# Kernel tuning notes

Hardware: AMD Instinct MI355X
Metric: run time of the kernel (lower is better)

Reference implementation:

```python
import jax, jax.numpy as jnp
import numpy as np

B, H, CI, O = 8, 16, 16, 16          # batch, child spatial, child caps, parent caps
K, S, ROUTINGS = 3, 1, 3             # kernel, stride, EM iterations
FINAL_LAMBDA = 0.01
EPS = 1e-9


def setup_inputs() -> dict:
    key = jax.random.key(0)
    k1, k2, k3, k4, k5 = jax.random.split(key, 5)
    inputs_pose = jax.random.normal(k1, (B, H, H, CI, 16), dtype=jnp.float32)
    inputs_activation = jax.random.uniform(k2, (B, H, H, CI, 1), dtype=jnp.float32)
    # transformation matrices: [1, k*k*child_caps, parent_caps, 4, 4]
    w = jax.random.normal(k3, (1, K * K * CI, O, 4, 4), dtype=jnp.float32)
    beta_a = jax.random.normal(k4, (O,), dtype=jnp.float32)
    beta_v = jax.random.normal(k5, (O,), dtype=jnp.float32)
    return {"inputs_pose": inputs_pose, "inputs_activation": inputs_activation,
            "w": w, "beta_a": beta_a, "beta_v": beta_v}


def _extract_patches(x, k, s):
    # kernel_tile: im2col-like gather. x: [B, H, W, ...] -> [B, p, p, k, k, ...]
    Hs = x.shape[1]
    p = (Hs - k) // s + 1
    idx = (jnp.arange(p) * s)[:, None] + jnp.arange(k)[None, :]      # [p, k]
    xh = x[:, idx]                   # [B, ph, kh, W, ...]
    patches = xh[:, :, :, idx]       # [B, ph, kh, pw, kw, ...]
    return jnp.swapaxes(patches, 2, 3), p


def _child_index_map(Hs, k, s, p):
    # flat child spatial index feeding each (parent pos, kernel slot)
    ph = np.arange(p)[:, None] * s + np.arange(k)[None, :]           # [p, k]
    ch = ph[:, None, :, None] * Hs + ph[None, :, None, :]            # [p, p, k, k]
    return ch.reshape(p * p, k * k)                                   # [P2, K2]


def reference(inputs_pose, inputs_activation, w, beta_a, beta_v):
    P = (H - K) // S + 1
    P2, K2 = P * P, K * K
    K2CI = K2 * CI

    # ---- kernel_tile ----
    pose_t, _ = _extract_patches(inputs_pose, K, S)       # [B,P,P,K,K,CI,16]
    act_t, _ = _extract_patches(inputs_activation, K, S)  # [B,P,P,K,K,CI,1]
    pose_unroll = pose_t.reshape(B * P2, K2CI, 4, 4)
    act_unroll = act_t.reshape(B * P2, K2CI)

    # ---- compute_votes: tiny 4x4 matmuls per (child slot, parent cap) ----
    votes = jnp.einsum('nkpq,koqr->nkopr', pose_unroll, w[0])  # [B*P2,K2CI,O,4,4]
    votes = votes.reshape(B, P2, K2CI, O, 16)
    act_i = act_unroll.reshape(B, P2, K2CI, 1, 1)

    # ---- spatial routing bookkeeping (static integers) ----
    child_idx = _child_index_map(H, K, S, P)                    # [P2, K2]
    kk_child = np.repeat(child_idx, CI, axis=1)                 # [P2, K2CI]
    counts = np.zeros(H * H, np.float32)
    np.add.at(counts, child_idx.reshape(-1), 1.0)               # parents per child pos
    cap_id = np.tile(np.arange(CI), K2)                         # [K2CI]
    seg = jnp.asarray((kk_child * CI + cap_id[None, :]).reshape(-1))  # [P2*K2CI]
    n_seg = H * H * CI

    # initial routing: uniform over all (parent pos, parent cap) each child feeds
    rr0 = 1.0 / (O * counts[kk_child])                          # [P2, K2CI]
    rr = jnp.asarray(rr0)[None, :, :, None, None]               # bcast [1,P2,K2CI,1,1]

    beta_a_b = beta_a.reshape(1, 1, 1, O, 1)
    beta_v_b = beta_v.reshape(1, 1, 1, O, 1)

    mean = act_j = None
    for it in range(ROUTINGS):
        inv_temp = FINAL_LAMBDA * (1.0 - 0.95 ** (it + 1))
        # ---- M-step: weighted Gaussian statistics ----
        rr_prime = rr * act_i                                   # [B,P2,K2CI,O,1]
        rr_sum = jnp.sum(rr_prime, axis=2, keepdims=True) + EPS # [B,P2,1,O,1]
        mean = jnp.sum(rr_prime * votes, axis=2, keepdims=True) / rr_sum
        var = jnp.sum(rr_prime * jnp.square(votes - mean), axis=2, keepdims=True) / rr_sum + EPS
        cost_h = (beta_v_b + 0.5 * jnp.log(var)) * rr_sum       # [B,P2,1,O,16]
        cost = jnp.sum(cost_h, axis=-1, keepdims=True)          # [B,P2,1,O,1]
        act_j = jax.nn.sigmoid(inv_temp * (beta_a_b - cost))    # [B,P2,1,O,1]
        # ---- E-step: softmax over all (parent pos, parent cap) per child capsule ----
        if it < ROUTINGS - 1:
            log_p = -0.5 * jnp.sum(jnp.square(votes - mean) / var
                                   + jnp.log(2.0 * np.pi * var), axis=-1)  # [B,P2,K2CI,O]
            zz = jnp.log(act_j[..., 0] + EPS) + log_p           # [B,P2,K2CI,O]
            z = jnp.transpose(zz, (1, 2, 0, 3)).reshape(P2 * K2CI, B, O)
            row_max = jnp.max(z, axis=-1)                       # [P2*K2CI, B]
            seg_max = jax.ops.segment_max(row_max, seg, num_segments=n_seg)
            g = seg_max[seg][..., None]
            ez = jnp.exp(z - g)
            denom = jax.ops.segment_sum(jnp.sum(ez, axis=-1), seg, num_segments=n_seg)[seg]
            rr_new = ez / (denom[..., None] + EPS)              # sums to 1 per child capsule
            rr = jnp.transpose(rr_new.reshape(P2, K2CI, B, O), (2, 0, 1, 3))[..., None]

    pose_out = mean[:, :, 0].reshape(B, P, P, O, 16)
    act_out = act_j[:, :, 0].reshape(B, P, P, O, 1)
    return pose_out, act_out
```

## Files before the change

kernel.cpp:

```cpp
#include <hip/hip_runtime.h>

namespace {
constexpr int B_ = 8, H_ = 16, CI_ = 16, O_ = 16, P_ = 14;
constexpr int P2_ = P_ * P_;
constexpr int K2CI_ = 144;
constexpr int NV_ = 2304;
constexpr float EPS_ = 1e-9f;
constexpr float LOG2PI_ = 1.8378770664093453f;

using f2 = __attribute__((ext_vector_type(2))) float;

__device__ __forceinline__ float cnt1(int h) {
  int lo = (h - (P_ - 1)) > 0 ? (h - (P_ - 1)) : 0;
  int hi = h < 2 ? h : 2;
  return (float)(hi - lo + 1);
}

__global__ __launch_bounds__(256) void transpose_w(const float* __restrict__ w,
                                                   float* __restrict__ wt) {
  const int i = blockIdx.x * 256 + threadIdx.x;
  const int ko = i >> 4, q = (i >> 2) & 3, r = i & 3;
  wt[(ko << 4) + (r << 2) + q] = w[i];
}

template <int MODE>
__global__ __launch_bounds__(512, 4) void caps_main(
    const float* __restrict__ pose, const float* __restrict__ act,
    const float* __restrict__ wt, const float* __restrict__ beta_a,
    const float* __restrict__ beta_v, const float* __restrict__ zin,
    const float* __restrict__ gmax, const float* __restrict__ gden,
    float* __restrict__ zout, float* __restrict__ out) {
  __shared__ __align__(16) float pose_s[NV_];
  __shared__ float rr_s[(MODE == 0) ? K2CI_ : NV_];
  __shared__ f2 partv[4][512];
  __shared__ float partr[512];
  __shared__ f2 sfin[4][64];
  __shared__ float sfr[64];
  __shared__ float gm_s[(MODE == 0) ? 1 : K2CI_];
  __shared__ float ad_s[(MODE == 0) ? 1 : K2CI_];

  const int tid = threadIdx.x;
  const int wv = __builtin_amdgcn_readfirstlane(tid >> 6);
  const int l = tid & 63;
  const int o = l >> 2, r = l & 3;
  const int pid = blockIdx.x;
  const int b = pid / P2_;
  const int p2 = pid - b * P2_;
  const int pi = p2 / P_;
  const int pj = p2 - pi * P_;
  const float inv_temp = (MODE == 0) ? 0.0005f : (MODE == 1) ? 0.000975f : 0.00142625f;

  if (tid < K2CI_) {
    const int ci = tid & 15, kk = tid >> 4;
    const int ki = (kk >= 6) ? 2 : (kk >= 3) ? 1 : 0, kj = kk - 3 * ki;
    const float* src = pose + ((size_t)((b * H_ + pi + ki) * H_ + pj + kj) << 8) + (ci << 4);
    const float4 R0 = *(const float4*)(src);
    const float4 R1 = *(const float4*)(src + 4);
    const float4 R2 = *(const float4*)(src + 8);
    const float4 R3 = *(const float4*)(src + 12);
    float4* dst = (float4*)(pose_s + (kk << 8) + (ci << 4));
    dst[0] = make_float4(R0.x, R1.x, R2.x, R3.x);
    dst[1] = make_float4(R0.y, R1.y, R2.y, R3.y);
    dst[2] = make_float4(R0.z, R1.z, R2.z, R3.z);
    dst[3] = make_float4(R0.w, R1.w, R2.w, R3.w);

    const int cidx = ((b * H_ + pi + ki) * H_ + pj + kj) * CI_ + ci;
    if (MODE == 0) {
      rr_s[tid] = act[cidx] / (16.0f * cnt1(pi + ki) * cnt1(pj + kj));
    } else {
      gm_s[tid] = gmax[cidx];
      ad_s[tid] = act[cidx] / (gden[cidx] + EPS_);
    }
  }
  if (MODE != 0) {
    __syncthreads();
    for (int i4 = tid; i4 < NV_ / 4; i4 += 512) {
      const float4 z4 = ((const float4*)(zin + (size_t)pid * NV_))[i4];
      const int k = i4 >> 2;
      const float gmk = gm_s[k], adk = ad_s[k];
      float4 r4;
      r4.x = __expf(z4.x - gmk) * adk;
      r4.y = __expf(z4.y - gmk) * adk;
      r4.z = __expf(z4.z - gmk) * adk;
      r4.w = __expf(z4.w - gmk) * adk;
      ((float4*)rr_s)[i4] = r4;
    }
  }
  __syncthreads();

  const float bvo = 16.0f * beta_v[o];
  const float bao = beta_a[o];

  const float* wt_l = wt + (l << 2);
  const int ci0 = wv * 2;

#define WT_OFF(idx) ((((idx) >> 1) << 12) + ((ci0 + ((idx)&1)) << 8))
#define PB_OFF(idx) ((((idx) >> 1) << 8) + ((ci0 + ((idx)&1)) << 4))

  f2 vc01[18], vc23[18];
  float prr = 0.f;
  f2 pm01 = {0.f, 0.f}, pm23 = {0.f, 0.f}, pv01 = {0.f, 0.f}, pv23 = {0.f, 0.f};
  {
    float4 wbuf0 = *(const float4*)(wt_l + WT_OFF(0));
    float4 wbuf1 = *(const float4*)(wt_l + WT_OFF(1));
#pragma unroll
    for (int idx = 0; idx < 18; ++idx) {
      const float4 w4 = (idx & 1) ? wbuf1 : wbuf0;
      if (idx < 16) {
        if (idx & 1)
          wbuf1 = *(const float4*)(wt_l + WT_OFF(idx + 2));
        else
          wbuf0 = *(const float4*)(wt_l + WT_OFF(idx + 2));
      }
      const float* pb = pose_s + PB_OFF(idx);
      const float4 P0 = *(const float4*)(pb);
      const float4 P1 = *(const float4*)(pb + 4);
      const float4 P2 = *(const float4*)(pb + 8);
      const float4 P3 = *(const float4*)(pb + 12);
      f2 v01 = (f2){P0.x, P0.y} * w4.x;
      f2 v23 = (f2){P0.z, P0.w} * w4.x;
      v01 = __builtin_elementwise_fma((f2){P1.x, P1.y}, (f2){w4.y, w4.y}, v01);
      v23 = __builtin_elementwise_fma((f2){P1.z, P1.w}, (f2){w4.y, w4.y}, v23);
      v01 = __builtin_elementwise_fma((f2){P2.x, P2.y}, (f2){w4.z, w4.z}, v01);
      v23 = __builtin_elementwise_fma((f2){P2.z, P2.w}, (f2){w4.z, w4.z}, v23);
      v01 = __builtin_elementwise_fma((f2){P3.x, P3.y}, (f2){w4.w, w4.w}, v01);
      v23 = __builtin_elementwise_fma((f2){P3.z, P3.w}, (f2){w4.w, w4.w}, v23);
      if (MODE != 2) {
        vc01[idx] = v01;
        vc23[idx] = v23;
      }
      const int k = ((idx >> 1) << 4) + ci0 + (idx & 1);
      const float rrk = (MODE == 0) ? rr_s[k] : rr_s[(k << 4) + o];
      prr += rrk;
      const f2 rr2 = {rrk, rrk};
      const f2 a01 = rr2 * v01, a23 = rr2 * v23;
      pm01 += a01;
      pm23 += a23;
      pv01 = __builtin_elementwise_fma(a01, v01, pv01);
      pv23 = __builtin_elementwise_fma(a23, v23, pv23);
    }
  }
  partv[0][tid] = pm01; partv[1][tid] = pm23;
  partv[2][tid] = pv01; partv[3][tid] = pv23;
  partr[tid] = prr;
  __syncthreads();
  if (tid < 320) {
    if (tid < 256) {
      const int st = tid >> 6, li = tid & 63;
      f2 acc = partv[st][li];
#pragma unroll
      for (int wvi = 1; wvi < 8; ++wvi) acc += partv[st][wvi * 64 + li];
      sfin[st][li] = acc;
    } else {
      const int li = tid & 63;
      float acc = partr[li];
#pragma unroll
      for (int wvi = 1; wvi < 8; ++wvi) acc += partr[wvi * 64 + li];
      sfr[li] = acc;
    }
  }
  __syncthreads();
  const f2 S01 = sfin[0][l], S23 = sfin[1][l];
  const f2 V01 = sfin[2][l], V23 = sfin[3][l];
  const float rsum = sfr[l] + EPS_;
  const float irs = 1.0f / rsum;
  const f2 irs2 = {irs, irs};
  const f2 m01 = S01 * irs2, m23 = S23 * irs2;
  const f2 zero2 = {0.f, 0.f}, eps2 = {EPS_, EPS_};
  const f2 va01 = __builtin_elementwise_max(V01 * irs2 - m01 * m01, zero2) + eps2;
  const f2 va23 = __builtin_elementwise_max(V23 * irs2 - m23 * m23, zero2) + eps2;
  float slv = __logf(va01.x) + __logf(va01.y) + __logf(va23.x) + __logf(va23.y);
  slv += __shfl_xor(slv, 1);
  slv += __shfl_xor(slv, 2);
  const float cost = (bvo + 0.5f * slv) * rsum;
  const float aj = 1.0f / (1.0f + __expf(-inv_temp * (bao - cost)));

  if (MODE == 2) {
    if (wv == 0) {
      float* ob = out + ((size_t)(pid * 16 + o) << 4) + r;
      ob[0] = m01.x; ob[4] = m01.y; ob[8] = m23.x; ob[12] = m23.y;
      if (r == 0) out[(size_t)B_ * P2_ * O_ * 16 + pid * 16 + o] = aj;
    }
    return;
  }

  const f2 iv01 = {1.0f / va01.x, 1.0f / va01.y};
  const f2 iv23 = {1.0f / va23.x, 1.0f / va23.y};
  const float Cz = __logf(aj + EPS_) - 0.5f * (slv + 16.0f * LOG2PI_);
  float* zo = zout + (size_t)pid * NV_ + o;
  {
#pragma unroll
    for (int idx = 0; idx < 18; ++idx) {
      const f2 d01 = vc01[idx] - m01, d23 = vc23[idx] - m23;
      const f2 q2 = __builtin_elementwise_fma(d01 * d01, iv01, (d23 * d23) * iv23);
      float q = q2.x + q2.y;
      q += __shfl_xor(q, 1);
      q += __shfl_xor(q, 2);
      const int k = ((idx >> 1) << 4) + ci0 + (idx & 1);
      if (r == 0) zo[k << 4] = Cz - 0.5f * q;
    }
  }
#undef WT_OFF
#undef PB_OFF
}

__global__ __launch_bounds__(256) void seg_reduce(const float* __restrict__ z,
                                                  float* __restrict__ gmax,
                                                  float* __restrict__ gden) {
  const int tid = blockIdx.x * 256 + threadIdx.x;
  const int part = tid & 3, ci = (tid >> 2) & 15, w2 = (tid >> 6) & 15;
  const int h = (tid >> 10) & 15, b = tid >> 14;
  float4 v[9];
  float m = -3.0e38f;
#pragma unroll
  for (int s = 0; s < 9; ++s) {
    const int ki = (s >= 6) ? 2 : (s >= 3) ? 1 : 0, kj = s - 3 * ki;
    const int pi = h - ki, pj = w2 - kj;
    if ((unsigned)pi < (unsigned)P_ && (unsigned)pj < (unsigned)P_) {
      v[s] = *(const float4*)(z + (size_t)(b * P2_ + pi * P_ + pj) * NV_ + s * 256 +
                              ci * 16 + part * 4);
    } else {
      v[s] = make_float4(-3.0e38f, -3.0e38f, -3.0e38f, -3.0e38f);
    }
    m = fmaxf(m, fmaxf(fmaxf(v[s].x, v[s].y), fmaxf(v[s].z, v[s].w)));
  }
  m = fmaxf(m, __shfl_xor(m, 1));
  m = fmaxf(m, __shfl_xor(m, 2));
  float s_ = 0.f;
#pragma unroll
  for (int s = 0; s < 9; ++s) {
    s_ += __expf(v[s].x - m) + __expf(v[s].y - m) + __expf(v[s].z - m) + __expf(v[s].w - m);
  }
  s_ += __shfl_xor(s_, 1);
  s_ += __shfl_xor(s_, 2);
  if (part == 0) {
    gmax[tid >> 2] = m;
    gden[tid >> 2] = s_;
  }
}
}

extern "C" void kernel_launch(void* const* d_in, const int* in_sizes, int n_in,
                              void* d_out, int out_size, void* d_ws, size_t ws_size,
                              hipStream_t stream) {
  const float* pose = (const float*)d_in[0];
  const float* act = (const float*)d_in[1];
  const float* w = (const float*)d_in[2];
  const float* ba = (const float*)d_in[3];
  const float* bv = (const float*)d_in[4];
  float* out = (float*)d_out;

  float* z = (float*)d_ws;
  float* gm = z + (size_t)B_ * P2_ * NV_;
  float* gd = gm + B_ * H_ * H_ * CI_;
  float* wt = gd + B_ * H_ * H_ * CI_;

  const int NB = B_ * P2_;
  transpose_w<<<144, 256, 0, stream>>>(w, wt);
  caps_main<0><<<NB, 512, 0, stream>>>(pose, act, wt, ba, bv, z, gm, gd, z, out);
  seg_reduce<<<512, 256, 0, stream>>>(z, gm, gd);
  caps_main<1><<<NB, 512, 0, stream>>>(pose, act, wt, ba, bv, z, gm, gd, z, out);
  seg_reduce<<<512, 256, 0, stream>>>(z, gm, gd);
  caps_main<2><<<NB, 512, 0, stream>>>(pose, act, wt, ba, bv, z, gm, gd, z, out);
}
```

Baseline: 153.6 us.

## Pre-transpose pose in global memory and read it directly instead of staging in LDS

Adds a pose transpose to the existing weight-transpose kernel so the 4x4 pose matrices are stored transposed in workspace once. The main kernels then drop the per-block LDS staging of the 3x3 patch and load pose directly from global memory (using an asm-forced VGPR offset so the loads stay per-lane vector loads). The weight prefetch is also deepened from two to four buffers. This removes the LDS footprint and the staging work at the cost of an extra global pass over pose and more global/cache traffic inside the inner loop.

```diff
diff --git a/kernel.cpp b/kernel.cpp
--- a/kernel.cpp
+++ b/kernel.cpp
@@ -3,6 +3,7 @@
 namespace {
 constexpr int B_ = 8, H_ = 16, CI_ = 16, O_ = 16, P_ = 14;
 constexpr int P2_ = P_ * P_;
+constexpr int NB_ = B_ * P2_;
 constexpr int K2CI_ = 144;
 constexpr int NV_ = 2304;
 constexpr float EPS_ = 1e-9f;
@@ -16,21 +17,29 @@
   return (float)(hi - lo + 1);
 }
 
-__global__ __launch_bounds__(256) void transpose_w(const float* __restrict__ w,
-                                                   float* __restrict__ wt) {
-  const int i = blockIdx.x * 256 + threadIdx.x;
-  const int ko = i >> 4, q = (i >> 2) & 3, r = i & 3;
-  wt[(ko << 4) + (r << 2) + q] = w[i];
+__global__ __launch_bounds__(256) void transpose_all(const float* __restrict__ pose,
+                                                     float* __restrict__ pose_t,
+                                                     const float* __restrict__ w,
+                                                     float* __restrict__ wt) {
+  if (blockIdx.x < 2048) {
+    const int i = blockIdx.x * 256 + threadIdx.x;
+    const int cell = i >> 4, idx = i & 15;
+    const int p = idx >> 2, q = idx & 3;
+    pose_t[(cell << 4) + (q << 2) + p] = pose[i];
+  } else {
+    const int i = (blockIdx.x - 2048) * 256 + threadIdx.x;
+    const int ko = i >> 4, q = (i >> 2) & 3, r = i & 3;
+    wt[(ko << 4) + (r << 2) + q] = w[i];
+  }
 }
 
 template <int MODE>
 __global__ __launch_bounds__(512, 4) void caps_main(
-    const float* __restrict__ pose, const float* __restrict__ act,
+    const float* __restrict__ pose_t, const float* __restrict__ act,
     const float* __restrict__ wt, const float* __restrict__ beta_a,
     const float* __restrict__ beta_v, const float* __restrict__ zin,
     const float* __restrict__ gmax, const float* __restrict__ gden,
     float* __restrict__ zout, float* __restrict__ out) {
-  __shared__ __align__(16) float pose_s[NV_];
   __shared__ float rr_s[(MODE == 0) ? K2CI_ : NV_];
   __shared__ f2 partv[4][512];
   __shared__ float partr[512];
@@ -53,17 +62,6 @@
   if (tid < K2CI_) {
     const int ci = tid & 15, kk = tid >> 4;
     const int ki = (kk >= 6) ? 2 : (kk >= 3) ? 1 : 0, kj = kk - 3 * ki;
-    const float* src = pose + ((size_t)((b * H_ + pi + ki) * H_ + pj + kj) << 8) + (ci << 4);
-    const float4 R0 = *(const float4*)(src);
-    const float4 R1 = *(const float4*)(src + 4);
-    const float4 R2 = *(const float4*)(src + 8);
-    const float4 R3 = *(const float4*)(src + 12);
-    float4* dst = (float4*)(pose_s + (kk << 8) + (ci << 4));
-    dst[0] = make_float4(R0.x, R1.x, R2.x, R3.x);
-    dst[1] = make_float4(R0.y, R1.y, R2.y, R3.y);
-    dst[2] = make_float4(R0.z, R1.z, R2.z, R3.z);
-    dst[3] = make_float4(R0.w, R1.w, R2.w, R3.w);
-
     const int cidx = ((b * H_ + pi + ki) * H_ + pj + kj) * CI_ + ci;
     if (MODE == 0) {
       rr_s[tid] = act[cidx] / (16.0f * cnt1(pi + ki) * cnt1(pj + kj));
@@ -91,28 +89,27 @@
   const float bvo = 16.0f * beta_v[o];
   const float bao = beta_a[o];
 
+  int vofs;
+  asm volatile("v_mov_b32 %0, 0" : "=v"(vofs));
+  const float* pose_b = pose_t + ((size_t)((b * H_ + pi) * H_ + pj) << 8) + vofs;
   const float* wt_l = wt + (l << 2);
   const int ci0 = wv * 2;
 
 #define WT_OFF(idx) ((((idx) >> 1) << 12) + ((ci0 + ((idx)&1)) << 8))
-#define PB_OFF(idx) ((((idx) >> 1) << 8) + ((ci0 + ((idx)&1)) << 4))
+#define PB_OFF(idx) (((((idx) >> 1) / 3) << 12) + ((((idx) >> 1) % 3) << 8) + ((ci0 + ((idx)&1)) << 4))
 
   f2 vc01[18], vc23[18];
   float prr = 0.f;
   f2 pm01 = {0.f, 0.f}, pm23 = {0.f, 0.f}, pv01 = {0.f, 0.f}, pv23 = {0.f, 0.f};
   {
-    float4 wbuf0 = *(const float4*)(wt_l + WT_OFF(0));
-    float4 wbuf1 = *(const float4*)(wt_l + WT_OFF(1));
+    float4 wbuf[4];
+#pragma unroll
+    for (int j = 0; j < 4; ++j) wbuf[j] = *(const float4*)(wt_l + WT_OFF(j));
 #pragma unroll
     for (int idx = 0; idx < 18; ++idx) {
-      const float4 w4 = (idx & 1) ? wbuf1 : wbuf0;
-      if (idx < 16) {
-        if (idx & 1)
-          wbuf1 = *(const float4*)(wt_l + WT_OFF(idx + 2));
-        else
-          wbuf0 = *(const float4*)(wt_l + WT_OFF(idx + 2));
-      }
-      const float* pb = pose_s + PB_OFF(idx);
+      const float4 w4 = wbuf[idx & 3];
+      if (idx < 14) wbuf[idx & 3] = *(const float4*)(wt_l + WT_OFF(idx + 4));
+      const float* pb = pose_b + PB_OFF(idx);
       const float4 P0 = *(const float4*)(pb);
       const float4 P1 = *(const float4*)(pb + 4);
       const float4 P2 = *(const float4*)(pb + 8);
@@ -251,15 +248,15 @@
   float* out = (float*)d_out;
 
   float* z = (float*)d_ws;
-  float* gm = z + (size_t)B_ * P2_ * NV_;
+  float* gm = z + (size_t)NB_ * NV_;
   float* gd = gm + B_ * H_ * H_ * CI_;
   float* wt = gd + B_ * H_ * H_ * CI_;
-
-  const int NB = B_ * P2_;
-  transpose_w<<<144, 256, 0, stream>>>(w, wt);
-  caps_main<0><<<NB, 512, 0, stream>>>(pose, act, wt, ba, bv, z, gm, gd, z, out);
+  float* pt = wt + 36864;
+
+  transpose_all<<<2192, 256, 0, stream>>>(pose, pt, w, wt);
+  caps_main<0><<<NB_, 512, 0, stream>>>(pt, act, wt, ba, bv, z, gm, gd, z, out);
   seg_reduce<<<512, 256, 0, stream>>>(z, gm, gd);
-  caps_main<1><<<NB, 512, 0, stream>>>(pose, act, wt, ba, bv, z, gm, gd, z, out);
+  caps_main<1><<<NB_, 512, 0, stream>>>(pt, act, wt, ba, bv, z, gm, gd, z, out);
   seg_reduce<<<512, 256, 0, stream>>>(z, gm, gd);
-  caps_main<2><<<NB, 512, 0, stream>>>(pose, act, wt, ba, bv, z, gm, gd, z, out);
-}
+  caps_main<2><<<NB_, 512, 0, stream>>>(pt, act, wt, ba, bv, z, gm, gd, z, out);
+}
```

Result: slower. 212.8 us (+38.6%).

## Fuse all routing stages into one cooperative persistent kernel with grid syncs

Applied to the files above, without the earlier changes.

Merges the weight transpose, three EM routing passes and two segment reductions into a single cooperative kernel. Stages are separated by grid.sync instead of kernel launches, and blocks loop persistently over parent positions. This removes launch gaps between six kernels. In exchange it adds grid-wide barrier cost, sizes shared memory for the worst case across all modes, and may lower occupancy because the grid is capped by the co-resident block count.

```diff
diff --git a/kernel.cpp b/kernel.cpp
--- a/kernel.cpp
+++ b/kernel.cpp
@@ -1,14 +1,30 @@
 #include <hip/hip_runtime.h>
+#include <hip/hip_cooperative_groups.h>
+
+namespace cg = cooperative_groups;
 
 namespace {
 constexpr int B_ = 8, H_ = 16, CI_ = 16, O_ = 16, P_ = 14;
 constexpr int P2_ = P_ * P_;
+constexpr int NB_ = B_ * P2_;
 constexpr int K2CI_ = 144;
 constexpr int NV_ = 2304;
+constexpr int NSEG_ = B_ * H_ * H_ * CI_;
 constexpr float EPS_ = 1e-9f;
 constexpr float LOG2PI_ = 1.8378770664093453f;
 
 using f2 = __attribute__((ext_vector_type(2))) float;
+
+struct __align__(16) Smem {
+  float pose_s[NV_];
+  float rr_s[NV_];
+  f2 partv[4][512];
+  float partr[512];
+  f2 sfin[4][64];
+  float sfr[64];
+  float gm_s[K2CI_];
+  float ad_s[K2CI_];
+};
 
 __device__ __forceinline__ float cnt1(int h) {
   int lo = (h - (P_ - 1)) > 0 ? (h - (P_ - 1)) : 0;
@@ -16,34 +32,17 @@
   return (float)(hi - lo + 1);
 }
 
-__global__ __launch_bounds__(256) void transpose_w(const float* __restrict__ w,
-                                                   float* __restrict__ wt) {
-  const int i = blockIdx.x * 256 + threadIdx.x;
-  const int ko = i >> 4, q = (i >> 2) & 3, r = i & 3;
-  wt[(ko << 4) + (r << 2) + q] = w[i];
-}
-
 template <int MODE>
-__global__ __launch_bounds__(512, 4) void caps_main(
+__device__ __forceinline__ void caps_body(
+    const int pid, const int tid, Smem& sm,
     const float* __restrict__ pose, const float* __restrict__ act,
     const float* __restrict__ wt, const float* __restrict__ beta_a,
-    const float* __restrict__ beta_v, const float* __restrict__ zin,
+    const float* __restrict__ beta_v, float* __restrict__ z,
     const float* __restrict__ gmax, const float* __restrict__ gden,
-    float* __restrict__ zout, float* __restrict__ out) {
-  __shared__ __align__(16) float pose_s[NV_];
-  __shared__ float rr_s[(MODE == 0) ? K2CI_ : NV_];
-  __shared__ f2 partv[4][512];
-  __shared__ float partr[512];
-  __shared__ f2 sfin[4][64];
-  __shared__ float sfr[64];
-  __shared__ float gm_s[(MODE == 0) ? 1 : K2CI_];
-  __shared__ float ad_s[(MODE == 0) ? 1 : K2CI_];
-
-  const int tid = threadIdx.x;
+    float* __restrict__ out) {
   const int wv = __builtin_amdgcn_readfirstlane(tid >> 6);
   const int l = tid & 63;
   const int o = l >> 2, r = l & 3;
-  const int pid = blockIdx.x;
   const int b = pid / P2_;
   const int p2 = pid - b * P2_;
   const int pi = p2 / P_;
@@ -58,7 +57,7 @@
     const float4 R1 = *(const float4*)(src + 4);
     const float4 R2 = *(const float4*)(src + 8);
     const float4 R3 = *(const float4*)(src + 12);
-    float4* dst = (float4*)(pose_s + (kk << 8) + (ci << 4));
+    float4* dst = (float4*)(sm.pose_s + (kk << 8) + (ci << 4));
     dst[0] = make_float4(R0.x, R1.x, R2.x, R3.x);
     dst[1] = make_float4(R0.y, R1.y, R2.y, R3.y);
     dst[2] = make_float4(R0.z, R1.z, R2.z, R3.z);
@@ -66,24 +65,24 @@
 
     const int cidx = ((b * H_ + pi + ki) * H_ + pj + kj) * CI_ + ci;
     if (MODE == 0) {
-      rr_s[tid] = act[cidx] / (16.0f * cnt1(pi + ki) * cnt1(pj + kj));
+      sm.rr_s[tid] = act[cidx] / (16.0f * cnt1(pi + ki) * cnt1(pj + kj));
     } else {
-      gm_s[tid] = gmax[cidx];
-      ad_s[tid] = act[cidx] / (gden[cidx] + EPS_);
+      sm.gm_s[tid] = gmax[cidx];
+      sm.ad_s[tid] = act[cidx] / (gden[cidx] + EPS_);
     }
   }
   if (MODE != 0) {
     __syncthreads();
     for (int i4 = tid; i4 < NV_ / 4; i4 += 512) {
-      const float4 z4 = ((const float4*)(zin + (size_t)pid * NV_))[i4];
+      const float4 z4 = ((const float4*)(z + (size_t)pid * NV_))[i4];
       const int k = i4 >> 2;
-      const float gmk = gm_s[k], adk = ad_s[k];
+      const float gmk = sm.gm_s[k], adk = sm.ad_s[k];
       float4 r4;
       r4.x = __expf(z4.x - gmk) * adk;
       r4.y = __expf(z4.y - gmk) * adk;
       r4.z = __expf(z4.z - gmk) * adk;
       r4.w = __expf(z4.w - gmk) * adk;
-      ((float4*)rr_s)[i4] = r4;
+      ((float4*)sm.rr_s)[i4] = r4;
     }
   }
   __syncthreads();
@@ -112,7 +111,7 @@
         else
           wbuf0 = *(const float4*)(wt_l + WT_OFF(idx + 2));
       }
-      const float* pb = pose_s + PB_OFF(idx);
+      const float* pb = sm.pose_s + PB_OFF(idx);
       const float4 P0 = *(const float4*)(pb);
       const float4 P1 = *(const float4*)(pb + 4);
       const float4 P2 = *(const float4*)(pb + 8);
@@ -130,7 +129,7 @@
         vc23[idx] = v23;
       }
       const int k = ((idx >> 1) << 4) + ci0 + (idx & 1);
-      const float rrk = (MODE == 0) ? rr_s[k] : rr_s[(k << 4) + o];
+      const float rrk = (MODE == 0) ? sm.rr_s[k] : sm.rr_s[(k << 4) + o];
       prr += rrk;
       const f2 rr2 = {rrk, rrk};
       const f2 a01 = rr2 * v01, a23 = rr2 * v23;
@@ -140,29 +139,29 @@
       pv23 = __builtin_elementwise_fma(a23, v23, pv23);
     }
   }
-  partv[0][tid] = pm01; partv[1][tid] = pm23;
-  partv[2][tid] = pv01; partv[3][tid] = pv23;
-  partr[tid] = prr;
+  sm.partv[0][tid] = pm01; sm.partv[1][tid] = pm23;
+  sm.partv[2][tid] = pv01; sm.partv[3][tid] = pv23;
+  sm.partr[tid] = prr;
   __syncthreads();
   if (tid < 320) {
     if (tid < 256) {
       const int st = tid >> 6, li = tid & 63;
-      f2 acc = partv[st][li];
-#pragma unroll
-      for (int wvi = 1; wvi < 8; ++wvi) acc += partv[st][wvi * 64 + li];
-      sfin[st][li] = acc;
+      f2 acc = sm.partv[st][li];
+#pragma unroll
+      for (int wvi = 1; wvi < 8; ++wvi) acc += sm.partv[st][wvi * 64 + li];
+      sm.sfin[st][li] = acc;
     } else {
       const int li = tid & 63;
-      float acc = partr[li];
-#pragma unroll
-      for (int wvi = 1; wvi < 8; ++wvi) acc += partr[wvi * 64 + li];
-      sfr[li] = acc;
+      float acc = sm.partr[li];
+#pragma unroll
+      for (int wvi = 1; wvi < 8; ++wvi) acc += sm.partr[wvi * 64 + li];
+      sm.sfr[li] = acc;
     }
   }
   __syncthreads();
-  const f2 S01 = sfin[0][l], S23 = sfin[1][l];
-  const f2 V01 = sfin[2][l], V23 = sfin[3][l];
-  const float rsum = sfr[l] + EPS_;
+  const f2 S01 = sm.sfin[0][l], S23 = sm.sfin[1][l];
+  const f2 V01 = sm.sfin[2][l], V23 = sm.sfin[3][l];
+  const float rsum = sm.sfr[l] + EPS_;
   const float irs = 1.0f / rsum;
   const f2 irs2 = {irs, irs};
   const f2 m01 = S01 * irs2, m23 = S23 * irs2;
@@ -181,14 +180,11 @@
       ob[0] = m01.x; ob[4] = m01.y; ob[8] = m23.x; ob[12] = m23.y;
       if (r == 0) out[(size_t)B_ * P2_ * O_ * 16 + pid * 16 + o] = aj;
     }
-    return;
-  }
-
-  const f2 iv01 = {1.0f / va01.x, 1.0f / va01.y};
-  const f2 iv23 = {1.0f / va23.x, 1.0f / va23.y};
-  const float Cz = __logf(aj + EPS_) - 0.5f * (slv + 16.0f * LOG2PI_);
-  float* zo = zout + (size_t)pid * NV_ + o;
-  {
+  } else {
+    const f2 iv01 = {1.0f / va01.x, 1.0f / va01.y};
+    const f2 iv23 = {1.0f / va23.x, 1.0f / va23.y};
+    const float Cz = __logf(aj + EPS_) - 0.5f * (slv + 16.0f * LOG2PI_);
+    float* zo = z + (size_t)pid * NV_ + o;
 #pragma unroll
     for (int idx = 0; idx < 18; ++idx) {
       const f2 d01 = vc01[idx] - m01, d23 = vc23[idx] - m23;
@@ -204,38 +200,88 @@
 #undef PB_OFF
 }
 
-__global__ __launch_bounds__(256) void seg_reduce(const float* __restrict__ z,
-                                                  float* __restrict__ gmax,
-                                                  float* __restrict__ gden) {
-  const int tid = blockIdx.x * 256 + threadIdx.x;
-  const int part = tid & 3, ci = (tid >> 2) & 15, w2 = (tid >> 6) & 15;
-  const int h = (tid >> 10) & 15, b = tid >> 14;
-  float4 v[9];
-  float m = -3.0e38f;
-#pragma unroll
-  for (int s = 0; s < 9; ++s) {
-    const int ki = (s >= 6) ? 2 : (s >= 3) ? 1 : 0, kj = s - 3 * ki;
-    const int pi = h - ki, pj = w2 - kj;
-    if ((unsigned)pi < (unsigned)P_ && (unsigned)pj < (unsigned)P_) {
-      v[s] = *(const float4*)(z + (size_t)(b * P2_ + pi * P_ + pj) * NV_ + s * 256 +
-                              ci * 16 + part * 4);
-    } else {
-      v[s] = make_float4(-3.0e38f, -3.0e38f, -3.0e38f, -3.0e38f);
-    }
-    m = fmaxf(m, fmaxf(fmaxf(v[s].x, v[s].y), fmaxf(v[s].z, v[s].w)));
-  }
-  m = fmaxf(m, __shfl_xor(m, 1));
-  m = fmaxf(m, __shfl_xor(m, 2));
-  float s_ = 0.f;
-#pragma unroll
-  for (int s = 0; s < 9; ++s) {
-    s_ += __expf(v[s].x - m) + __expf(v[s].y - m) + __expf(v[s].z - m) + __expf(v[s].w - m);
-  }
-  s_ += __shfl_xor(s_, 1);
-  s_ += __shfl_xor(s_, 2);
-  if (part == 0) {
-    gmax[tid >> 2] = m;
-    gden[tid >> 2] = s_;
+__device__ __forceinline__ void seg_body(const int gtid, const int gstride,
+                                         const float* __restrict__ z,
+                                         float* __restrict__ gmax,
+                                         float* __restrict__ gden) {
+  for (int t = gtid; t < NSEG_ * 4; t += gstride) {
+    const int part = t & 3, ci = (t >> 2) & 15, w2 = (t >> 6) & 15;
+    const int h = (t >> 10) & 15, b = t >> 14;
+    float4 v[9];
+    float m = -3.0e38f;
+#pragma unroll
+    for (int s = 0; s < 9; ++s) {
+      const int ki = (s >= 6) ? 2 : (s >= 3) ? 1 : 0, kj = s - 3 * ki;
+      const int pi = h - ki, pj = w2 - kj;
+      if ((unsigned)pi < (unsigned)P_ && (unsigned)pj < (unsigned)P_) {
+        v[s] = *(const float4*)(z + (size_t)(b * P2_ + pi * P_ + pj) * NV_ + s * 256 +
+                                ci * 16 + part * 4);
+      } else {
+        v[s] = make_float4(-3.0e38f, -3.0e38f, -3.0e38f, -3.0e38f);
+      }
+      m = fmaxf(m, fmaxf(fmaxf(v[s].x, v[s].y), fmaxf(v[s].z, v[s].w)));
+    }
+    m = fmaxf(m, __shfl_xor(m, 1));
+    m = fmaxf(m, __shfl_xor(m, 2));
+    float s_ = 0.f;
+#pragma unroll
+    for (int s = 0; s < 9; ++s) {
+      s_ += __expf(v[s].x - m) + __expf(v[s].y - m) + __expf(v[s].z - m) + __expf(v[s].w - m);
+    }
+    s_ += __shfl_xor(s_, 1);
+    s_ += __shfl_xor(s_, 2);
+    if (part == 0) {
+      gmax[t >> 2] = m;
+      gden[t >> 2] = s_;
+    }
+  }
+}
+
+__global__ __launch_bounds__(512, 4) void caps_fused(
+    const float* __restrict__ pose, const float* __restrict__ act,
+    const float* __restrict__ w, const float* __restrict__ beta_a,
+    const float* __restrict__ beta_v, float* __restrict__ z,
+    float* __restrict__ gm, float* __restrict__ gd,
+    float* __restrict__ wt, float* __restrict__ out) {
+  __shared__ Smem sm;
+  const int tid = threadIdx.x;
+  cg::grid_group grid = cg::this_grid();
+  const int G = gridDim.x;
+  const int gtid = blockIdx.x * 512 + tid;
+  const int gstride = G * 512;
+
+  for (int i = gtid; i < K2CI_ * O_ * 16; i += gstride) {
+    const int ko = i >> 4, q = (i >> 2) & 3, r = i & 3;
+    wt[(ko << 4) + (r << 2) + q] = w[i];
+  }
+  __threadfence();
+  grid.sync();
+
+  for (int pid = blockIdx.x; pid < NB_; pid += G) {
+    caps_body<0>(pid, tid, sm, pose, act, wt, beta_a, beta_v, z, gm, gd, out);
+    __syncthreads();
+  }
+  __threadfence();
+  grid.sync();
+
+  seg_body(gtid, gstride, z, gm, gd);
+  __threadfence();
+  grid.sync();
+
+  for (int pid = blockIdx.x; pid < NB_; pid += G) {
+    caps_body<1>(pid, tid, sm, pose, act, wt, beta_a, beta_v, z, gm, gd, out);
+    __syncthreads();
+  }
+  __threadfence();
+  grid.sync();
+
+  seg_body(gtid, gstride, z, gm, gd);
+  __threadfence();
+  grid.sync();
+
+  for (int pid = blockIdx.x; pid < NB_; pid += G) {
+    caps_body<2>(pid, tid, sm, pose, act, wt, beta_a, beta_v, z, gm, gd, out);
+    __syncthreads();
   }
 }
 }
@@ -251,15 +297,18 @@
   float* out = (float*)d_out;
 
   float* z = (float*)d_ws;
-  float* gm = z + (size_t)B_ * P2_ * NV_;
+  float* gm = z + (size_t)NB_ * NV_;
   float* gd = gm + B_ * H_ * H_ * CI_;
   float* wt = gd + B_ * H_ * H_ * CI_;
 
-  const int NB = B_ * P2_;
-  transpose_w<<<144, 256, 0, stream>>>(w, wt);
-  caps_main<0><<<NB, 512, 0, stream>>>(pose, act, wt, ba, bv, z, gm, gd, z, out);
-  seg_reduce<<<512, 256, 0, stream>>>(z, gm, gd);
-  caps_main<1><<<NB, 512, 0, stream>>>(pose, act, wt, ba, bv, z, gm, gd, z, out);
-  seg_reduce<<<512, 256, 0, stream>>>(z, gm, gd);
-  caps_main<2><<<NB, 512, 0, stream>>>(pose, act, wt, ba, bv, z, gm, gd, z, out);
-}
+  int bpc = 0;
+  if (hipOccupancyMaxActiveBlocksPerMultiprocessor(&bpc, caps_fused, 512, 0) != hipSuccess ||
+      bpc < 1)
+    bpc = 1;
+  int G = bpc * 256;
+  if (G > NB_) G = NB_;
+
+  void* args[] = {(void*)&pose, (void*)&act, (void*)&w,  (void*)&ba, (void*)&bv,
+                  (void*)&z,    (void*)&gm,  (void*)&gd, (void*)&wt, (void*)&out};
+  hipLaunchCooperativeKernel(caps_fused, dim3(G), dim3(512), args, 0, stream);
+}
```

Result: slower. 555.2 us (+261.6%).
